# Kernel tuning notes

Hardware: AMD Instinct MI355X
Metric: run time of the kernel (lower is better)

The kernel has to match this reference:

```python
import jax, jax.numpy as jnp
from jax import lax
import numpy as np

H = W = 512
P = 8            # points_per_pixel
DIM = 16         # args.dim
NPTS = 100000    # point cloud size (range of idbufs)
HID = 256        # radiance-mapping MLP hidden width
TOTAL = H * W * P


def setup_inputs() -> dict:
    key = jax.random.key(0)
    ks = jax.random.split(key, 24)
    zbufs = jax.random.normal(ks[0], (H, W, P), dtype=jnp.float32)  # ~half > 0 -> pixel_mask
    idbufs = jax.random.randint(ks[1], (H, W, P), 0, NPTS)
    o = jnp.array([0.1, -0.2, 0.3], dtype=jnp.float32)
    dirs = jax.random.normal(ks[2], (H, W, 3), dtype=jnp.float32)
    dirs = dirs / jnp.linalg.norm(dirs, axis=-1, keepdims=True)
    cos = 0.5 + 0.5 * jax.random.uniform(ks[3], (H, W, 1), dtype=jnp.float32)  # keep away from 0
    ray = jnp.concatenate([jnp.broadcast_to(o, (H, W, 3)), dirs, cos], axis=-1)  # [H,W,7]
    gt = jax.random.uniform(ks[4], (H, W, 3), dtype=jnp.float32)
    mask_gt = jnp.ones((H, W, 1), dtype=jnp.float32)
    xyz_o = jax.random.normal(ks[5], (NPTS, 3), dtype=jnp.float32)
    s = 0.05
    params = {
        'mlp_w1': s * jax.random.normal(ks[6], (6, HID), dtype=jnp.float32),
        'mlp_b1': jnp.zeros((HID,), dtype=jnp.float32),
        'mlp_w2': s * jax.random.normal(ks[7], (HID, DIM), dtype=jnp.float32),
        'mlp_b2': jnp.zeros((DIM,), dtype=jnp.float32),
        'mpn_w1': s * jax.random.normal(ks[8], (3, 3, P * DIM, P * DIM), dtype=jnp.float32),
        'mpn_b1': jnp.zeros((P * DIM,), dtype=jnp.float32),
        'mpn_w2': s * jax.random.normal(ks[9], (3, 3, P * DIM, P * DIM), dtype=jnp.float32),
        'mpn_b2': jnp.zeros((P * DIM,), dtype=jnp.float32),
        'unet_w1': s * jax.random.normal(ks[10], (3, 3, P * DIM, 64), dtype=jnp.float32),
        'unet_b1': jnp.zeros((64,), dtype=jnp.float32),
        'unet_w2': s * jax.random.normal(ks[11], (3, 3, 64, 3), dtype=jnp.float32),
        'unet_b2': jnp.zeros((3,), dtype=jnp.float32),
    }
    return dict(zbufs=zbufs, idbufs=idbufs, ray=ray, gt=gt, mask_gt=mask_gt,
                isTrain=0, xyz_o=xyz_o, **params)


def _conv(x, w, b):
    return lax.conv_general_dilated(x, w, (1, 1), 'SAME',
                                    dimension_numbers=('NHWC', 'HWIO', 'NHWC')) + b


def reference(zbufs, idbufs, ray, gt, mask_gt, isTrain, xyz_o,
              mlp_w1, mlp_b1, mlp_w2, mlp_b2,
              mpn_w1, mpn_b1, mpn_w2, mpn_b2,
              unet_w1, unet_b1, unet_w2, unet_b2):
    thresh = 0.2 if isTrain else 0.0
    o = ray[0, 0, :3]                   # camera origin (constant over image)
    dirs = ray[..., 3:6]                # [H,W,3]
    cos = ray[..., 6]                   # [H,W]

    mask = (zbufs > thresh).reshape(-1)        # [TOTAL] pixel_mask
    ids = idbufs.reshape(-1)                   # [TOTAL] point ids

    # torch.unique + stable argsort + cumsum(counts) selects, per unique id,
    # the FIRST masked occurrence in flat order -> fixed-shape segment_min.
    order = jnp.arange(TOTAL, dtype=jnp.int32)
    seg = jnp.where(mask, ids, 0)
    vals = jnp.where(mask, order, TOTAL)
    first = jax.ops.segment_min(vals, seg, num_segments=NPTS)   # [NPTS]
    first_idx = jnp.clip(first, 0, TOTAL - 1)

    pix = first_idx // P                                        # pixel of first occurrence
    z_u = zbufs.reshape(-1)[first_idx]                          # [NPTS]
    cos_u = cos.reshape(-1)[pix]                                # [NPTS]
    d_u = dirs.reshape(-1, 3)[pix]                              # [NPTS,3]
    xyz_u = o + (z_u / cos_u)[:, None] * d_u                    # [NPTS,3]

    # radiance-mapping MLP on unique points
    h = jax.nn.relu(jnp.concatenate([xyz_u, d_u], axis=-1) @ mlp_w1 + mlp_b1)
    feat = h @ mlp_w2 + mlp_b2                                  # [NPTS,DIM]

    # scatter features back: feature_map[pixel_mask] = feature[inverse_indices]
    fm = jnp.where(mask[:, None], feat[ids], 0.0)               # [TOTAL,DIM]
    x = fm.reshape(1, H, W, P * DIM)                            # NHWC

    # MPN_tiny: predict per-channel mask
    m = jax.nn.sigmoid(_conv(jax.nn.relu(_conv(x, mpn_w1, mpn_b1)), mpn_w2, mpn_b2))
    fused = x * m

    # UNet refinement (stand-in)
    u = jax.nn.relu(_conv(fused, unet_w1, unet_b1))
    img = _conv(u, unet_w2, unet_b2)[0]                         # [H,W,3]
    return img
```

## Files before the change

kernel.cpp:

```cpp
#include <hip/hip_runtime.h>

#define HH 512
#define WW 512
#define PP 8
#define NPTS 100000
#define HID 256
#define TOTAL (HH*WW*PP)

typedef _Float16 f16x8 __attribute__((ext_vector_type(8)));
typedef float    f32x4 __attribute__((ext_vector_type(4)));

__global__ void k_init_first(int* first) {
    int i = blockIdx.x*256 + threadIdx.x;
    if (i < NPTS) first[i] = 0x7FFFFFFF;
}

__global__ void k_segmin(const float* __restrict__ z, const int* __restrict__ ids,
                         const int* __restrict__ isTrain, int* __restrict__ first) {
    int i = blockIdx.x*256 + threadIdx.x;
    float thr = (*isTrain) ? 0.2f : 0.0f;
    if (z[i] > thr) atomicMin(&first[ids[i]], i);
}

__global__ void k_mlp(const int* __restrict__ first, const float* __restrict__ z,
                      const float* __restrict__ ray,
                      const float* __restrict__ w1, const float* __restrict__ b1,
                      const float* __restrict__ w2, const float* __restrict__ b2,
                      float* __restrict__ feat) {
    int j = blockIdx.x*256 + threadIdx.x;
    if (j >= NPTS) return;
    int fi = first[j];
    fi = min(fi, TOTAL-1);
    int pix = fi >> 3;
    float zv = z[fi];
    float ox = ray[0], oy = ray[1], oz = ray[2];
    const float* rp = ray + pix*7;
    float dx0 = rp[3], dy0 = rp[4], dz0 = rp[5], cs = rp[6];
    float tt = zv / cs;
    float in6[6] = { ox + tt*dx0, oy + tt*dy0, oz + tt*dz0, dx0, dy0, dz0 };
    float acc[16];
    #pragma unroll
    for (int o=0;o<16;o++) acc[o] = b2[o];
    for (int jh=0; jh<HID; ++jh) {
        float h = b1[jh];
        #pragma unroll
        for (int k=0;k<6;k++) h += in6[k]*w1[k*HID+jh];
        h = fmaxf(h, 0.0f);
        const float4* w2p = (const float4*)(w2 + jh*16);
        float4 q0 = w2p[0], q1 = w2p[1], q2 = w2p[2], q3 = w2p[3];
        acc[0]  += h*q0.x; acc[1]  += h*q0.y; acc[2]  += h*q0.z; acc[3]  += h*q0.w;
        acc[4]  += h*q1.x; acc[5]  += h*q1.y; acc[6]  += h*q1.z; acc[7]  += h*q1.w;
        acc[8]  += h*q2.x; acc[9]  += h*q2.y; acc[10] += h*q2.z; acc[11] += h*q2.w;
        acc[12] += h*q3.x; acc[13] += h*q3.y; acc[14] += h*q3.z; acc[15] += h*q3.w;
    }
    float4* fp = (float4*)(feat + j*16);
    fp[0] = make_float4(acc[0],acc[1],acc[2],acc[3]);
    fp[1] = make_float4(acc[4],acc[5],acc[6],acc[7]);
    fp[2] = make_float4(acc[8],acc[9],acc[10],acc[11]);
    fp[3] = make_float4(acc[12],acc[13],acc[14],acc[15]);
}

__global__ void k_gather(const float* __restrict__ z, const int* __restrict__ ids,
                         const int* __restrict__ isTrain,
                         const float* __restrict__ feat, _Float16* __restrict__ xh) {
    int i = blockIdx.x*256 + threadIdx.x;
    float thr = (*isTrain) ? 0.2f : 0.0f;
    bool m = z[i] > thr;
    float f[16];
    if (m) {
        const float4* fp = (const float4*)(feat + ids[i]*16);
        float4 v0=fp[0], v1=fp[1], v2=fp[2], v3=fp[3];
        f[0]=v0.x; f[1]=v0.y; f[2]=v0.z; f[3]=v0.w;
        f[4]=v1.x; f[5]=v1.y; f[6]=v1.z; f[7]=v1.w;
        f[8]=v2.x; f[9]=v2.y; f[10]=v2.z; f[11]=v2.w;
        f[12]=v3.x; f[13]=v3.y; f[14]=v3.z; f[15]=v3.w;
    } else {
        #pragma unroll
        for (int j=0;j<16;j++) f[j]=0.f;
    }
    f16x8 h0, h1;
    #pragma unroll
    for (int j=0;j<8;j++){ h0[j]=(_Float16)f[j]; h1[j]=(_Float16)f[j+8]; }
    *(f16x8*)(xh + (size_t)i*16)     = h0;
    *(f16x8*)(xh + (size_t)i*16 + 8) = h1;
}

__global__ void k_wcvt(const float* __restrict__ w, _Float16* __restrict__ wt, int COUT) {
    int i = blockIdx.x*256 + threadIdx.x;
    if (i >= 9*128*COUT) return;
    int co = i % COUT; int tmp = i / COUT;
    int ci = tmp & 127; int tt = tmp >> 7;
    wt[((size_t)(tt*4 + (ci>>5))*COUT + co)*32 + (ci&31)] = (_Float16)w[i];
}

template<int COUT, int ACT>
__global__ __launch_bounds__(256, 2)
void k_convmfma(const _Float16* __restrict__ in, const _Float16* __restrict__ wt,
                const float* __restrict__ bias, const _Float16* aux,
                _Float16* __restrict__ out)
{
    constexpr int FN = COUT/32;
    __shared__ __align__(16) _Float16 smem[23040];
    int t = threadIdx.x;
    int bx = blockIdx.x & 31, by = blockIdx.x >> 5;
    int x0 = bx*16, y0 = by*8;

    for (int u = t; u < 2880; u += 256) {
        int pix = u >> 4, slot = u & 15;
        int yn = pix / 18, xn = pix - yn*18;
        int gy = y0 + yn - 1, gx = x0 + xn - 1;
        uint4 v = make_uint4(0u,0u,0u,0u);
        if (gy >= 0 && gy < HH && gx >= 0 && gx < WW)
            v = *(const uint4*)(in + ((size_t)(gy*WW+gx))*128 + slot*8);
        int ps = slot ^ (xn & 7);
        *(uint4*)(&smem[pix*128 + ps*8]) = v;
    }
    __syncthreads();

    int lane = t & 63, wid = t >> 6;
    int wm = wid >> 1, wn = wid & 1;
    int lx = lane & 15, sg = lane >> 4;

    f32x4 acc[4][FN];
    #pragma unroll
    for (int i=0;i<4;i++)
        #pragma unroll
        for (int j=0;j<FN;j++) acc[i][j] = (f32x4){0.f,0.f,0.f,0.f};

    const _Float16* wbase = wt + (size_t)(wn*(COUT/2) + lx)*32 + sg*8;

    #pragma unroll 1
    for (int dy=0; dy<3; ++dy) {
        #pragma unroll
        for (int dx=0; dx<3; ++dx) {
            int tt = dy*3+dx;
            int xn = lx + dx;
            int xk = xn & 7;
            #pragma unroll
            for (int cc=0; cc<4; ++cc) {
                f16x8 b[FN];
                #pragma unroll
                for (int fn=0; fn<FN; ++fn)
                    b[fn] = *(const f16x8*)(wbase + (size_t)((tt*4+cc)*COUT + fn*16)*32);
                #pragma unroll
                for (int fm=0; fm<4; ++fm) {
                    int yn = wm*4 + fm + dy;
                    int slot = (cc*4 + sg) ^ xk;
                    f16x8 a = *(const f16x8*)(&smem[((yn*18 + xn)*16 + slot)*8]);
                    #pragma unroll
                    for (int fn=0; fn<FN; ++fn)
                        acc[fm][fn] = __builtin_amdgcn_mfma_f32_16x16x32_f16(a, b[fn], acc[fm][fn], 0,0,0);
                }
            }
        }
    }
    __syncthreads();

    #pragma unroll
    for (int fm=0; fm<4; ++fm) {
        int y = wm*4 + fm;
        #pragma unroll
        for (int fn=0; fn<FN; ++fn) {
            int cout = wn*(COUT/2) + fn*16 + lx;
            float bb = bias[cout];
            #pragma unroll
            for (int r=0; r<4; ++r) {
                int x = sg*4 + r;
                float v = acc[fm][fn][r] + bb;
                float res;
                if (ACT == 0) {
                    res = fmaxf(v, 0.f);
                } else {
                    float xa = (float)aux[((size_t)((y0+y)*WW + x0+x))*128 + cout];
                    res = xa / (1.f + __expf(-v));
                }
                smem[(y*16 + x)*COUT + cout] = (_Float16)res;
            }
        }
    }
    __syncthreads();

    constexpr int UNITS = 128*COUT/8;
    for (int u = t; u < UNITS; u += 256) {
        int byte = u*16;
        int y = byte / (16*COUT*2);
        int rest = byte - y*(16*COUT*2);
        uint4 v = *(const uint4*)((const char*)smem + byte);
        *(uint4*)((char*)out + ((size_t)((y0+y)*WW + x0)*COUT)*2 + rest) = v;
    }
}

__global__ __launch_bounds__(256)
void k_conv4(const _Float16* __restrict__ u, const float* __restrict__ w,
             const float* __restrict__ bias, float* __restrict__ out) {
    int pix = blockIdx.x*256 + threadIdx.x;
    int y = pix >> 9, x = pix & 511;
    float a0 = bias[0], a1 = bias[1], a2 = bias[2];
    for (int dy=0; dy<3; ++dy) {
        int gy = y + dy - 1;
        if (gy < 0 || gy >= HH) continue;
        for (int dx=0; dx<3; ++dx) {
            int gx = x + dx - 1;
            if (gx < 0 || gx >= WW) continue;
            const _Float16* ip = u + (size_t)(gy*WW+gx)*64;
            const float* wp = w + (dy*3+dx)*192;
            #pragma unroll
            for (int c8=0; c8<8; ++c8) {
                f16x8 v = *(const f16x8*)(ip + c8*8);
                #pragma unroll
                for (int e=0; e<8; ++e) {
                    float f = (float)v[e];
                    const float* q = wp + (c8*8+e)*3;
                    a0 += f*q[0]; a1 += f*q[1]; a2 += f*q[2];
                }
            }
        }
    }
    float* op = out + (size_t)pix*3;
    op[0]=a0; op[1]=a1; op[2]=a2;
}

extern "C" void kernel_launch(void* const* d_in, const int* in_sizes, int n_in,
                              void* d_out, int out_size, void* d_ws, size_t ws_size,
                              hipStream_t stream) {
    const float* zbufs = (const float*)d_in[0];
    const int*   idb   = (const int*)d_in[1];
    const float* ray   = (const float*)d_in[2];
    const int*   isTr  = (const int*)d_in[5];
    const float* mlp_w1 = (const float*)d_in[7];
    const float* mlp_b1 = (const float*)d_in[8];
    const float* mlp_w2 = (const float*)d_in[9];
    const float* mlp_b2 = (const float*)d_in[10];
    const float* mpn_w1 = (const float*)d_in[11];
    const float* mpn_b1 = (const float*)d_in[12];
    const float* mpn_w2 = (const float*)d_in[13];
    const float* mpn_b2 = (const float*)d_in[14];
    const float* un_w1  = (const float*)d_in[15];
    const float* un_b1  = (const float*)d_in[16];
    const float* un_w2  = (const float*)d_in[17];
    const float* un_b2  = (const float*)d_in[18];

    char* ws = (char*)d_ws;
    _Float16* bufXh = (_Float16*)(ws);
    _Float16* bufT  = (_Float16*)(ws + (size_t)64*1024*1024);
    _Float16* bufF  = (_Float16*)(ws + (size_t)128*1024*1024);
    char* sc = ws + (size_t)192*1024*1024;
    int*      first = (int*)(sc);
    float*    feat  = (float*)(sc + (size_t)1*1024*1024);
    _Float16* wt1   = (_Float16*)(sc + (size_t)8*1024*1024);
    _Float16* wt2   = (_Float16*)(sc + (size_t)9*1024*1024);
    _Float16* wt3   = (_Float16*)(sc + (size_t)10*1024*1024);
    float* img = (float*)d_out;

    hipLaunchKernelGGL(k_init_first, dim3((NPTS+255)/256), dim3(256), 0, stream, first);
    hipLaunchKernelGGL(k_segmin, dim3(TOTAL/256), dim3(256), 0, stream, zbufs, idb, isTr, first);
    hipLaunchKernelGGL(k_mlp, dim3((NPTS+255)/256), dim3(256), 0, stream,
                       first, zbufs, ray, mlp_w1, mlp_b1, mlp_w2, mlp_b2, feat);
    hipLaunchKernelGGL(k_wcvt, dim3((9*128*128+255)/256), dim3(256), 0, stream, mpn_w1, wt1, 128);
    hipLaunchKernelGGL(k_wcvt, dim3((9*128*128+255)/256), dim3(256), 0, stream, mpn_w2, wt2, 128);
    hipLaunchKernelGGL(k_wcvt, dim3((9*128*64+255)/256), dim3(256), 0, stream, un_w1, wt3, 64);
    hipLaunchKernelGGL(k_gather, dim3(TOTAL/256), dim3(256), 0, stream,
                       zbufs, idb, isTr, feat, bufXh);
    hipLaunchKernelGGL((k_convmfma<128,0>), dim3(2048), dim3(256), 0, stream,
                       bufXh, wt1, mpn_b1, (const _Float16*)nullptr, bufT);
    hipLaunchKernelGGL((k_convmfma<128,1>), dim3(2048), dim3(256), 0, stream,
                       bufT, wt2, mpn_b2, bufXh, bufF);
    hipLaunchKernelGGL((k_convmfma<64,0>), dim3(2048), dim3(256), 0, stream,
                       bufF, wt3, un_b1, (const _Float16*)nullptr, bufT);
    hipLaunchKernelGGL(k_conv4, dim3(TOTAL/PP/256), dim3(256), 0, stream,
                       bufT, un_w2, un_b2, img);
}
```

Measured before the change: 560.2 us.

## Use direct global-to-LDS loads, swap MFMA operands, write conv outputs from registers

The conv tile halo is now loaded with global_load_lds straight into shared memory, and out-of-bounds pixels read from a zero pad buffer instead of branching. The swizzle is inverted on the source side. The MFMA operands are swapped so each lane holds 4 consecutive output channels, which lets the epilogue write f16x4 directly to global memory without staging through LDS and without two syncthreads. Launch bounds are raised to 3 blocks per CU. The risks are narrower global stores, register pressure under the tighter occupancy target, and the extra zpad buffer that has to be initialised.

```diff
diff --git a/kernel.cpp b/kernel.cpp
--- a/kernel.cpp
+++ b/kernel.cpp
@@ -8,11 +8,15 @@
 #define TOTAL (HH*WW*PP)
 
 typedef _Float16 f16x8 __attribute__((ext_vector_type(8)));
+typedef _Float16 f16x4 __attribute__((ext_vector_type(4)));
 typedef float    f32x4 __attribute__((ext_vector_type(4)));
-
-__global__ void k_init_first(int* first) {
+typedef __attribute__((address_space(1))) const unsigned int gu32;
+typedef __attribute__((address_space(3))) unsigned int lu32;
+
+__global__ void k_init_first(int* first, float4* zpad) {
     int i = blockIdx.x*256 + threadIdx.x;
     if (i < NPTS) first[i] = 0x7FFFFFFF;
+    if (i < 64) zpad[i] = make_float4(0.f,0.f,0.f,0.f);
 }
 
 __global__ void k_segmin(const float* __restrict__ z, const int* __restrict__ ids,
@@ -94,10 +98,10 @@
 }
 
 template<int COUT, int ACT>
-__global__ __launch_bounds__(256, 2)
+__global__ __launch_bounds__(256, 3)
 void k_convmfma(const _Float16* __restrict__ in, const _Float16* __restrict__ wt,
                 const float* __restrict__ bias, const _Float16* aux,
-                _Float16* __restrict__ out)
+                _Float16* __restrict__ out, const _Float16* __restrict__ zpad)
 {
     constexpr int FN = COUT/32;
     __shared__ __align__(16) _Float16 smem[23040];
@@ -106,14 +110,14 @@
     int x0 = bx*16, y0 = by*8;
 
     for (int u = t; u < 2880; u += 256) {
-        int pix = u >> 4, slot = u & 15;
+        int pix = u >> 4, p = u & 15;
         int yn = pix / 18, xn = pix - yn*18;
         int gy = y0 + yn - 1, gx = x0 + xn - 1;
-        uint4 v = make_uint4(0u,0u,0u,0u);
-        if (gy >= 0 && gy < HH && gx >= 0 && gx < WW)
-            v = *(const uint4*)(in + ((size_t)(gy*WW+gx))*128 + slot*8);
-        int ps = slot ^ (xn & 7);
-        *(uint4*)(&smem[pix*128 + ps*8]) = v;
+        int slot = p ^ (xn & 7);
+        const _Float16* src = (gy >= 0 && gy < HH && gx >= 0 && gx < WW)
+            ? in + ((size_t)(gy*WW+gx))*128 + slot*8
+            : zpad;
+        __builtin_amdgcn_global_load_lds((gu32*)src, (lu32*)&smem[u*8], 16, 0, 0);
     }
     __syncthreads();
 
@@ -140,53 +144,43 @@
             for (int cc=0; cc<4; ++cc) {
                 f16x8 b[FN];
                 #pragma unroll
-                for (int fn=0; fn<FN; ++fn)
-                    b[fn] = *(const f16x8*)(wbase + (size_t)((tt*4+cc)*COUT + fn*16)*32);
-                #pragma unroll
-                for (int fm=0; fm<4; ++fm) {
-                    int yn = wm*4 + fm + dy;
+                for (int cf=0; cf<FN; ++cf)
+                    b[cf] = *(const f16x8*)(wbase + (size_t)((tt*4+cc)*COUT + cf*16)*32);
+                #pragma unroll
+                for (int yy=0; yy<4; ++yy) {
+                    int yn = wm*4 + yy + dy;
                     int slot = (cc*4 + sg) ^ xk;
                     f16x8 a = *(const f16x8*)(&smem[((yn*18 + xn)*16 + slot)*8]);
                     #pragma unroll
-                    for (int fn=0; fn<FN; ++fn)
-                        acc[fm][fn] = __builtin_amdgcn_mfma_f32_16x16x32_f16(a, b[fn], acc[fm][fn], 0,0,0);
+                    for (int cf=0; cf<FN; ++cf)
+                        acc[yy][cf] = __builtin_amdgcn_mfma_f32_16x16x32_f16(b[cf], a, acc[yy][cf], 0,0,0);
                 }
             }
         }
     }
-    __syncthreads();
-
-    #pragma unroll
-    for (int fm=0; fm<4; ++fm) {
-        int y = wm*4 + fm;
-        #pragma unroll
-        for (int fn=0; fn<FN; ++fn) {
-            int cout = wn*(COUT/2) + fn*16 + lx;
-            float bb = bias[cout];
-            #pragma unroll
-            for (int r=0; r<4; ++r) {
-                int x = sg*4 + r;
-                float v = acc[fm][fn][r] + bb;
-                float res;
-                if (ACT == 0) {
-                    res = fmaxf(v, 0.f);
-                } else {
-                    float xa = (float)aux[((size_t)((y0+y)*WW + x0+x))*128 + cout];
-                    res = xa / (1.f + __expf(-v));
+
+    #pragma unroll
+    for (int yy=0; yy<4; ++yy) {
+        int gy = y0 + wm*4 + yy;
+        size_t prow = ((size_t)gy*WW + x0 + lx);
+        #pragma unroll
+        for (int cf=0; cf<FN; ++cf) {
+            int c0 = wn*(COUT/2) + cf*16 + sg*4;
+            f16x4 v;
+            if (ACT == 0) {
+                #pragma unroll
+                for (int r=0;r<4;r++)
+                    v[r] = (_Float16)fmaxf(acc[yy][cf][r] + bias[c0+r], 0.f);
+            } else {
+                f16x4 av = *(const f16x4*)(aux + prow*128 + c0);
+                #pragma unroll
+                for (int r=0;r<4;r++) {
+                    float s = acc[yy][cf][r] + bias[c0+r];
+                    v[r] = (_Float16)((float)av[r] / (1.f + __expf(-s)));
                 }
-                smem[(y*16 + x)*COUT + cout] = (_Float16)res;
             }
+            *(f16x4*)(out + prow*COUT + c0) = v;
         }
-    }
-    __syncthreads();
-
-    constexpr int UNITS = 128*COUT/8;
-    for (int u = t; u < UNITS; u += 256) {
-        int byte = u*16;
-        int y = byte / (16*COUT*2);
-        int rest = byte - y*(16*COUT*2);
-        uint4 v = *(const uint4*)((const char*)smem + byte);
-        *(uint4*)((char*)out + ((size_t)((y0+y)*WW + x0)*COUT)*2 + rest) = v;
     }
 }
 
@@ -250,9 +244,10 @@
     _Float16* wt1   = (_Float16*)(sc + (size_t)8*1024*1024);
     _Float16* wt2   = (_Float16*)(sc + (size_t)9*1024*1024);
     _Float16* wt3   = (_Float16*)(sc + (size_t)10*1024*1024);
+    float4*   zpad  = (float4*)(sc + (size_t)11*1024*1024);
     float* img = (float*)d_out;
 
-    hipLaunchKernelGGL(k_init_first, dim3((NPTS+255)/256), dim3(256), 0, stream, first);
+    hipLaunchKernelGGL(k_init_first, dim3((NPTS+255)/256), dim3(256), 0, stream, first, zpad);
     hipLaunchKernelGGL(k_segmin, dim3(TOTAL/256), dim3(256), 0, stream, zbufs, idb, isTr, first);
     hipLaunchKernelGGL(k_mlp, dim3((NPTS+255)/256), dim3(256), 0, stream,
                        first, zbufs, ray, mlp_w1, mlp_b1, mlp_w2, mlp_b2, feat);
@@ -262,11 +257,11 @@
     hipLaunchKernelGGL(k_gather, dim3(TOTAL/256), dim3(256), 0, stream,
                        zbufs, idb, isTr, feat, bufXh);
     hipLaunchKernelGGL((k_convmfma<128,0>), dim3(2048), dim3(256), 0, stream,
-                       bufXh, wt1, mpn_b1, (const _Float16*)nullptr, bufT);
+                       bufXh, wt1, mpn_b1, (const _Float16*)nullptr, bufT, (const _Float16*)zpad);
     hipLaunchKernelGGL((k_convmfma<128,1>), dim3(2048), dim3(256), 0, stream,
-                       bufT, wt2, mpn_b2, bufXh, bufF);
+                       bufT, wt2, mpn_b2, bufXh, bufF, (const _Float16*)zpad);
     hipLaunchKernelGGL((k_convmfma<64,0>), dim3(2048), dim3(256), 0, stream,
-                       bufF, wt3, un_b1, (const _Float16*)nullptr, bufT);
+                       bufF, wt3, un_b1, (const _Float16*)nullptr, bufT, (const _Float16*)zpad);
     hipLaunchKernelGGL(k_conv4, dim3(TOTAL/PP/256), dim3(256), 0, stream,
                        bufT, un_w2, un_b2, img);
 }
```

After: 538.0 us. 4.0% less time.
